# Kernel optimization log

Measured on AMD Instinct MI355X. Metric: run time of the kernel, lower is better.

Reference implementation:

```python
import jax, jax.numpy as jnp
import numpy as np

B, N, D, E = 64, 512, 256, 128   # batch, n_nodes, node_model_dim, edge_model_dim
N_ITERS = 20                      # max_iter_sinkhorn with fixed_n_iters=True


def setup_inputs() -> dict:
    key = jax.random.key(0)
    ks = jax.random.split(key, 9)
    return {
        "node_embeddings_inputs": jax.random.normal(ks[0], (B, N, D), jnp.float32),
        "node_masks_inputs": jax.random.randint(ks[1], (B, N), 0, 2).astype(bool),
        "node_embeddings_outputs": jax.random.normal(ks[2], (B, N, D), jnp.float32),
        # learned parameters
        "node_padding_features": jax.random.normal(ks[3], (1, 1, D), jnp.float32),
        "positional_encoding_outputs": jax.random.normal(ks[4], (1, N, D), jnp.float32),
        # stand-in for the (externally defined) EvoformerSetMatching pair stack:
        # a bilinear pair-affinity head, followed by the module's own linear_aff
        "W_a": jax.random.normal(ks[5], (D, E), jnp.float32) / np.sqrt(D),
        "W_b": jax.random.normal(ks[6], (D, E), jnp.float32) / np.sqrt(D),
        "w_aff": jax.random.normal(ks[7], (E,), jnp.float32) / np.sqrt(E),  # linear_aff weight
        "b_aff": jnp.zeros((), jnp.float32),                                # linear_aff bias
    }


def _sinkhorn(K, n_iters):
    # Fixed-iteration Sinkhorn projection toward a doubly-stochastic matrix:
    # alternately normalize columns (dim=2 sums) and rows (dim=1 sums).
    def step(P, _):
        P = P / jnp.sum(P, axis=2, keepdims=True)  # row-normalize over inputs axis
        P = P / jnp.sum(P, axis=1, keepdims=True)  # col-normalize over outputs axis
        return P, None
    P, _ = jax.lax.scan(step, K, None, length=n_iters)
    return P


def reference(node_embeddings_inputs, node_masks_inputs, node_embeddings_outputs,
              node_padding_features, positional_encoding_outputs,
              W_a, W_b, w_aff, b_aff):
    # replace padded input nodes with the learned padding feature
    mask = node_masks_inputs[..., None]                              # [B, N, 1]
    x_in = jnp.where(mask, node_padding_features, node_embeddings_inputs)
    # add positional encoding to output nodes (add_positionnal_outputs=True)
    x_out = node_embeddings_outputs + positional_encoding_outputs

    # pairwise affinity: aff[b, i(out), j(in)]  (linear_aff fused into the contraction
    # so the [B,N,N,E] pair tensor is never materialized)
    a = (x_out @ W_a) * w_aff                                        # [B, N, E]
    b = x_in @ W_b                                                   # [B, N, E]
    aff = jnp.einsum('bie,bje->bij', a, b) + b_aff                   # [B, N, N]

    # approximate doubly-stochastic init: average of the two marginal softmaxes
    K = 0.5 * jax.nn.softmax(aff, axis=1) + 0.5 * jax.nn.softmax(aff, axis=2)
    return _sinkhorn(K, N_ITERS)
```

## Files before the change

kernel.cpp:

```cpp
#include <hip/hip_runtime.h>
#include <cstddef>

static constexpr int CB = 64;
static constexpr int CN = 512;
static constexpr int CD = 256;
static constexpr int CE = 128;
static constexpr int CIT = 20;

typedef _Float16 half_t;
typedef __attribute__((ext_vector_type(8))) _Float16 v8h;
typedef __attribute__((ext_vector_type(4))) _Float16 v4h;
typedef __attribute__((ext_vector_type(4))) float v4f;

__global__ __launch_bounds__(512) void k0_init(
    const void* __restrict__ mask, int* __restrict__ flag,
    const float* __restrict__ W_a, const float* __restrict__ W_b,
    const float* __restrict__ w_aff,
    half_t* __restrict__ WaF, half_t* __restrict__ WbF,
    float4* __restrict__ clearp, int nclear4) {
  const int tid = threadIdx.x;
  const int blk = blockIdx.x;
  if (blk == 1) return;
  if (blk >= 18) {
    const int idx = (blk - 18) * 512 + tid;
    if (idx < nclear4)
      clearp[idx] = make_float4(-1.0f, -1.0f, -1.0f, -1.0f);
    return;
  }
  if (blk >= 2) {
    const bool is_a = (blk < 10);
    const float* W = is_a ? W_a : W_b;
    half_t* WF = is_a ? WaF : WbF;
    const int e = (blk - (is_a ? 2 : 10)) * 512 + tid;
    const int fB = e >> 6, lane = e & 63;
    const int nn = fB >> 3, kf = fB & 7;
    const int col = nn * 16 + (lane & 15);
    const int q = lane >> 4;
    const float scale = is_a ? w_aff[col] : 1.0f;
    v8h hv;
#pragma unroll
    for (int j = 0; j < 8; ++j) {
      const int k = kf * 32 + q * 8 + j;
      hv[j] = (half_t)(W[(size_t)k * CE + col] * scale);
    }
    *(v8h*)&WF[(size_t)e * 8] = hv;
    return;
  }
  __shared__ int cnt[5];
  if (tid < 5) cnt[tid] = 0;
  __syncthreads();
  const unsigned char* p = (const unsigned char*)mask;
  int l0 = 0, l1 = 0, l2 = 0, l3 = 0, l4 = 0;
  const int base = tid * 64;
  for (int k = 0; k < 64; ++k) {
    const int off = base + k;
    if (p[off]) {
      const int m4 = off & 3;
      if (m4 == 1) l1++;
      else if (m4 == 2) l2++;
      else if (m4 == 3) l3++;
      else if ((off & 7) == 4) l4++;
      else l0++;
    }
  }
  if (l0) atomicAdd(&cnt[0], 1);
  if (l1) atomicAdd(&cnt[1], 1);
  if (l2) atomicAdd(&cnt[2], 1);
  if (l3) atomicAdd(&cnt[3], 1);
  if (l4) atomicAdd(&cnt[4], 1);
  __syncthreads();
  if (tid == 0) {
    int f;
    if (cnt[1]) f = 1;
    else if (cnt[2] || cnt[3]) f = 2;
    else if (cnt[4]) f = 0;
    else if (cnt[0]) f = 3;
    else f = 1;
    *flag = f;
  }
}

__global__ __launch_bounds__(256) void prep_both(
    const float* __restrict__ out_emb, const float* __restrict__ pos,
    const float* __restrict__ in_emb, const float* __restrict__ pad,
    const void* __restrict__ maskp, const int* __restrict__ flagp,
    const half_t* __restrict__ WaF, const half_t* __restrict__ WbF,
    half_t* __restrict__ A_h, half_t* __restrict__ Bm_h) {
  __shared__ half_t Xs[64][264];
  const int tid = threadIdx.x;
  const int wv = tid >> 6, ln = tid & 63;
  const bool isA = blockIdx.x < 512;
  const int row0 = (isA ? blockIdx.x : blockIdx.x - 512) * 64;
  const float* X = isA ? out_emb : in_emb;
  const float* extra = isA ? pos : pad;
  const half_t* Wfrag = isA ? WaF : WbF;
  half_t* out = isA ? A_h : Bm_h;
  const int flag = isA ? 0 : *flagp;

#pragma unroll 4
  for (int it = 0; it < 16; ++it) {
    const int r = it * 4 + wv;
    const int row = row0 + r;
    const int c = ln * 4;
    float4 x4;
    if (isA) {
      x4 = *(const float4*)&X[(size_t)row * CD + c];
      const int i = row & (CN - 1);
      const float4 p4 = *(const float4*)&extra[(size_t)i * CD + c];
      x4.x += p4.x; x4.y += p4.y; x4.z += p4.z; x4.w += p4.w;
    } else {
      bool m;
      if (flag == 1)      m = ((const unsigned char*)maskp)[row] != 0;
      else if (flag == 2) m = ((const float*)maskp)[row] != 0.0f;
      else if (flag == 3) m = ((const long long*)maskp)[row] != 0;
      else                m = ((const int*)maskp)[row] != 0;
      if (m) x4 = *(const float4*)&extra[c];
      else   x4 = *(const float4*)&X[(size_t)row * CD + c];
    }
    v4h hv;
    hv[0] = (half_t)x4.x; hv[1] = (half_t)x4.y;
    hv[2] = (half_t)x4.z; hv[3] = (half_t)x4.w;
    *(v4h*)&Xs[r][c] = hv;
  }
  __syncthreads();

  const int q = ln >> 4, l = ln & 15;
  v8h af[8];
#pragma unroll
  for (int kf = 0; kf < 8; ++kf)
    af[kf] = *(v8h*)&Xs[wv * 16 + l][kf * 32 + q * 8];
  v4f acc[8] = {};
#pragma unroll
  for (int nn = 0; nn < 8; ++nn) {
    v8h bf[8];
#pragma unroll
    for (int kf = 0; kf < 8; ++kf)
      bf[kf] = *(const v8h*)&Wfrag[(size_t)((nn * 8 + kf) * 64 + ln) * 8];
#pragma unroll
    for (int kf = 0; kf < 8; ++kf)
      acc[nn] = __builtin_amdgcn_mfma_f32_16x16x32_f16(af[kf], bf[kf], acc[nn], 0, 0, 0);
  }
#pragma unroll
  for (int nn = 0; nn < 8; ++nn)
#pragma unroll
    for (int g = 0; g < 4; ++g) {
      const int row = row0 + wv * 16 + q * 4 + g;
      out[(size_t)row * CE + nn * 16 + l] = (half_t)acc[nn][g];
    }
}

__global__ __launch_bounds__(512, 2) void fused_reg(
    const half_t* __restrict__ A_h, const half_t* __restrict__ B_h,
    const float* __restrict__ baff, float* __restrict__ P,
    float* __restrict__ partInit, float* __restrict__ partIter) {
  __shared__ float comb2[8][512][2];
  __shared__ float2 w12[512];
  __shared__ float csinv_l[512];
  __shared__ float rinv_l[128];

  const int tid = threadIdx.x;
  const int wv = tid >> 6, ln = tid & 63;
  const int q = ln >> 4, l = ln & 15;
  const int b = blockIdx.x & 63;
  const int slab = blockIdx.x >> 6;
  const int i0 = slab * 128;
  const float bbs = *baff - 2.7725887f;

  int rs3[3];
  {
    int k = 0;
#pragma unroll
    for (int sl = 0; sl < 4; ++sl)
      if (sl != slab) rs3[k++] = sl;
  }

  v8h af[4];
  {
    const half_t* Arow = &A_h[((size_t)b * CN + i0 + wv * 16 + l) * CE];
#pragma unroll
    for (int ki = 0; ki < 4; ++ki)
      af[ki] = *(const v8h*)&Arow[ki * 32 + q * 8];
  }
  float ef[32][4];
  float d[4] = {0.0f, 0.0f, 0.0f, 0.0f};
  const half_t* Bbase = &B_h[(size_t)b * CN * CE];
#pragma unroll
  for (int ct = 0; ct < 32; ++ct) {
    v8h bf[4];
    const half_t* Brow = &Bbase[(size_t)(ct * 16 + l) * CE];
#pragma unroll
    for (int ki = 0; ki < 4; ++ki)
      bf[ki] = *(const v8h*)&Brow[ki * 32 + q * 8];
    v4f acc = {};
#pragma unroll
    for (int ki = 0; ki < 4; ++ki)
      acc = __builtin_amdgcn_mfma_f32_16x16x32_f16(af[ki], bf[ki], acc, 0, 0, 0);
    float colsum = 0.0f;
#pragma unroll
    for (int g = 0; g < 4; ++g) {
      const float e = __expf(acc[g] + bbs);
      ef[ct][g] = e;
      d[g] += e;
      colsum += e;
    }
    colsum += __shfl_xor(colsum, 16);
    colsum += __shfl_xor(colsum, 32);
    if (ln < 16) comb2[wv][ct * 16 + ln][0] = colsum;
  }
#pragma unroll
  for (int g = 0; g < 4; ++g) {
#pragma unroll
    for (int m = 1; m < 16; m <<= 1) d[g] += __shfl_xor(d[g], m);
  }
  if (l == 0) {
#pragma unroll
    for (int g = 0; g < 4; ++g) rinv_l[wv * 16 + q * 4 + g] = 1.0f / d[g];
  }
  __syncthreads();

  {
    float S = 0.0f;
#pragma unroll
    for (int w = 0; w < 8; ++w) S += comb2[w][tid][0];
    float T = S;
    __hip_atomic_store(&partInit[(((size_t)b * 4 + slab) * 512) + tid], S,
                       __ATOMIC_RELAXED, __HIP_MEMORY_SCOPE_AGENT);
    float v0, v1, v2;
    float* pb = &partInit[(size_t)b * 4 * 512];
    while (true) {
      v0 = __hip_atomic_load(&pb[rs3[0] * 512 + tid], __ATOMIC_RELAXED, __HIP_MEMORY_SCOPE_AGENT);
      v1 = __hip_atomic_load(&pb[rs3[1] * 512 + tid], __ATOMIC_RELAXED, __HIP_MEMORY_SCOPE_AGENT);
      v2 = __hip_atomic_load(&pb[rs3[2] * 512 + tid], __ATOMIC_RELAXED, __HIP_MEMORY_SCOPE_AGENT);
      if (v0 > 0.0f && v1 > 0.0f && v2 > 0.0f) break;
      __builtin_amdgcn_s_sleep(1);
    }
    T += v0 + v1 + v2;
    const float ci = 1.0f / T;
    csinv_l[tid] = ci;
    w12[tid] = make_float2(0.5f * ci, 1.0f);
  }
  float rv[4];
#pragma unroll
  for (int g = 0; g < 4; ++g) rv[g] = rinv_l[wv * 16 + q * 4 + g];

  float u_[4], uri[4];
  for (int t = 0; t < CIT; ++t) {
    __syncthreads();
    float p1[4] = {0, 0, 0, 0}, p2[4] = {0, 0, 0, 0};
#pragma unroll
    for (int ct = 0; ct < 32; ++ct) {
      const float2 w = w12[ct * 16 + l];
#pragma unroll
      for (int g = 0; g < 4; ++g) {
        const float e = ef[ct][g];
        p1[g] = fmaf(e, w.x, p1[g]);
        p2[g] = fmaf(e, w.y, p2[g]);
      }
    }
#pragma unroll
    for (int g = 0; g < 4; ++g) {
#pragma unroll
      for (int m = 1; m < 16; m <<= 1) {
        p1[g] += __shfl_xor(p1[g], m);
        p2[g] += __shfl_xor(p2[g], m);
      }
      u_[g] = 1.0f / (p1[g] + 0.5f * rv[g] * p2[g]);
      uri[g] = u_[g] * rv[g];
    }
#pragma unroll
    for (int ct = 0; ct < 32; ++ct) {
      float s1 = 0.0f, s2 = 0.0f;
#pragma unroll
      for (int g = 0; g < 4; ++g) {
        const float e = ef[ct][g];
        s1 = fmaf(e, u_[g], s1);
        s2 = fmaf(e, uri[g], s2);
      }
      s1 += __shfl_xor(s1, 16);
      s2 += __shfl_xor(s2, 16);
      const float sel = (ln >= 32) ? s1 : s2;
      const float recv = __shfl_xor(sel, 32);
      const float z = ((ln < 32) ? s1 : s2) + recv;
      if ((ln & 16) == 0) comb2[wv][ct * 16 + (ln & 15)][ln >> 5] = z;
    }
    __syncthreads();
    float S1 = 0.0f, S2 = 0.0f;
#pragma unroll
    for (int w = 0; w < 8; ++w) {
      const float2 c2 = *(const float2*)&comb2[w][tid][0];
      S1 += c2.x;
      S2 += c2.y;
    }
    const float ci = csinv_l[tid];
    const float Q = 0.5f * fmaf(ci, S1, S2);
    float* pr = &partIter[(((size_t)t * 64 + b) * 4) * 512];
    __hip_atomic_store(&pr[slab * 512 + tid], Q,
                       __ATOMIC_RELAXED, __HIP_MEMORY_SCOPE_AGENT);
    float v0, v1, v2;
    while (true) {
      v0 = __hip_atomic_load(&pr[rs3[0] * 512 + tid], __ATOMIC_RELAXED, __HIP_MEMORY_SCOPE_AGENT);
      v1 = __hip_atomic_load(&pr[rs3[1] * 512 + tid], __ATOMIC_RELAXED, __HIP_MEMORY_SCOPE_AGENT);
      v2 = __hip_atomic_load(&pr[rs3[2] * 512 + tid], __ATOMIC_RELAXED, __HIP_MEMORY_SCOPE_AGENT);
      if (v0 > 0.0f && v1 > 0.0f && v2 > 0.0f) break;
      __builtin_amdgcn_s_sleep(1);
    }
    const float vv = 1.0f / (Q + v0 + v1 + v2);
    w12[tid] = make_float2(0.5f * vv * ci, vv);
  }

  __syncthreads();
  float* Pb = &P[((size_t)b * CN + i0 + wv * 16 + q * 4) * CN];
#pragma unroll
  for (int ct = 0; ct < 32; ++ct) {
    const float2 w = w12[ct * 16 + l];
    const float c1 = w.x;
    const float c2 = 0.5f * w.y;
#pragma unroll
    for (int g = 0; g < 4; ++g) {
      const float e = ef[ct][g];
      Pb[(size_t)g * CN + ct * 16 + l] = e * fmaf(u_[g], c1, uri[g] * c2);
    }
  }
}

extern "C" void kernel_launch(void* const* d_in, const int* in_sizes, int n_in,
                              void* d_out, int out_size, void* d_ws, size_t ws_size,
                              hipStream_t stream) {
  const float* in_emb  = (const float*)d_in[0];
  const void*  mask    = d_in[1];
  const float* out_emb = (const float*)d_in[2];
  const float* pad     = (const float*)d_in[3];
  const float* pos     = (const float*)d_in[4];
  const float* W_a     = (const float*)d_in[5];
  const float* W_b     = (const float*)d_in[6];
  const float* w_aff   = (const float*)d_in[7];
  const float* b_aff   = (const float*)d_in[8];
  float* P = (float*)d_out;

  char* ws = (char*)d_ws;
  const size_t MB = 1024 * 1024;
  half_t* A_h  = (half_t*)ws;
  half_t* Bm_h = (half_t*)(ws + 8 * MB);
  int*    flag = (int*)(ws + 16 * MB);
  half_t* WaF  = (half_t*)(ws + 16 * MB + 16384);
  half_t* WbF  = (half_t*)(ws + 16 * MB + 16384 + 65536);
  float* partInit = (float*)(ws + 16 * MB + 256 * 1024);
  float* partIter = (float*)(ws + 16 * MB + 768 * 1024);

  const int nclear4 = (512 * 1024 + 10 * 1024 * 1024) / 16;
  const int nclrblk = (nclear4 + 511) / 512;

  k0_init<<<dim3(18 + nclrblk), dim3(512), 0, stream>>>(
      mask, flag, W_a, W_b, w_aff, WaF, WbF, (float4*)partInit, nclear4);
  prep_both<<<dim3(1024), dim3(256), 0, stream>>>(
      out_emb, pos, in_emb, pad, mask, flag, WaF, WbF, A_h, Bm_h);
  fused_reg<<<dim3(256), dim3(512), 0, stream>>>(
      A_h, Bm_h, b_aff, P, partInit, partIter);
}
```

Measured before the change: 309.6 us.

## Store exp tile in fp16 and do Sinkhorn reductions with MFMA

Keeps the exponentiated affinity tile in registers as fp16, plus a transposed copy computed with a second MFMA. Row and column sums in the init and in each Sinkhorn iteration become matrix-vector MFMAs against fp16 scaling vectors, replacing scalar FMA loops and cross-lane shuffle reductions. This cuts VALU and shuffle work per iteration, and fp16 storage halves the register footprint for the tile. In exchange it doubles the init MFMAs, wastes most MFMA output lanes because the operand is effectively a vector, and rounds the tile and scaling factors to fp16, which can hurt accuracy.

```diff
diff --git a/kernel.cpp b/kernel.cpp
--- a/kernel.cpp
+++ b/kernel.cpp
@@ -156,7 +156,8 @@
   __shared__ float comb2[8][512][2];
   __shared__ float2 w12[512];
   __shared__ float csinv_l[512];
-  __shared__ float rinv_l[128];
+  __shared__ half_t w1h[512];
+  __shared__ half_t w2h[512];
 
   const int tid = threadIdx.x;
   const int wv = tid >> 6, ln = tid & 63;
@@ -181,8 +182,8 @@
     for (int ki = 0; ki < 4; ++ki)
       af[ki] = *(const v8h*)&Arow[ki * 32 + q * 8];
   }
-  float ef[32][4];
-  float d[4] = {0.0f, 0.0f, 0.0f, 0.0f};
+  v4h eh[32];
+  v4h ehT[32];
   const half_t* Bbase = &B_h[(size_t)b * CN * CE];
 #pragma unroll
   for (int ct = 0; ct < 32; ++ct) {
@@ -191,31 +192,33 @@
 #pragma unroll
     for (int ki = 0; ki < 4; ++ki)
       bf[ki] = *(const v8h*)&Brow[ki * 32 + q * 8];
-    v4f acc = {};
-#pragma unroll
-    for (int ki = 0; ki < 4; ++ki)
-      acc = __builtin_amdgcn_mfma_f32_16x16x32_f16(af[ki], bf[ki], acc, 0, 0, 0);
-    float colsum = 0.0f;
+    v4f acc = {}, accT = {};
+#pragma unroll
+    for (int ki = 0; ki < 4; ++ki) {
+      acc  = __builtin_amdgcn_mfma_f32_16x16x32_f16(af[ki], bf[ki], acc,  0, 0, 0);
+      accT = __builtin_amdgcn_mfma_f32_16x16x32_f16(bf[ki], af[ki], accT, 0, 0, 0);
+    }
 #pragma unroll
     for (int g = 0; g < 4; ++g) {
-      const float e = __expf(acc[g] + bbs);
-      ef[ct][g] = e;
-      d[g] += e;
-      colsum += e;
-    }
-    colsum += __shfl_xor(colsum, 16);
-    colsum += __shfl_xor(colsum, 32);
-    if (ln < 16) comb2[wv][ct * 16 + ln][0] = colsum;
-  }
-#pragma unroll
-  for (int g = 0; g < 4; ++g) {
-#pragma unroll
-    for (int m = 1; m < 16; m <<= 1) d[g] += __shfl_xor(d[g], m);
-  }
-  if (l == 0) {
-#pragma unroll
-    for (int g = 0; g < 4; ++g) rinv_l[wv * 16 + q * 4 + g] = 1.0f / d[g];
-  }
+      eh[ct][g]  = (half_t)__expf(acc[g]  + bbs);
+      ehT[ct][g] = (half_t)__expf(accT[g] + bbs);
+    }
+  }
+
+  v4h ones;
+  ones[0] = (half_t)1.0f; ones[1] = (half_t)1.0f;
+  ones[2] = (half_t)1.0f; ones[3] = (half_t)1.0f;
+  v4f rowacc = {};
+#pragma unroll
+  for (int ct = 0; ct < 32; ++ct) {
+    const v4f c0 = __builtin_amdgcn_mfma_f32_16x16x16f16(ones, eh[ct], (v4f){}, 0, 0, 0);
+    if (ln < 16) comb2[wv][ct * 16 + ln][0] = c0[0];
+    rowacc = __builtin_amdgcn_mfma_f32_16x16x16f16(ones, ehT[ct], rowacc, 0, 0, 0);
+  }
+  float rv[4];
+#pragma unroll
+  for (int g = 0; g < 4; ++g)
+    rv[g] = 1.0f / __shfl(rowacc[0], q * 4 + g);
   __syncthreads();
 
   {
@@ -238,50 +241,36 @@
     const float ci = 1.0f / T;
     csinv_l[tid] = ci;
     w12[tid] = make_float2(0.5f * ci, 1.0f);
-  }
-  float rv[4];
-#pragma unroll
-  for (int g = 0; g < 4; ++g) rv[g] = rinv_l[wv * 16 + q * 4 + g];
+    w1h[tid] = (half_t)(0.5f * ci);
+    w2h[tid] = (half_t)1.0f;
+  }
 
   float u_[4], uri[4];
   for (int t = 0; t < CIT; ++t) {
     __syncthreads();
-    float p1[4] = {0, 0, 0, 0}, p2[4] = {0, 0, 0, 0};
+    v4f P1 = {}, P2 = {};
 #pragma unroll
     for (int ct = 0; ct < 32; ++ct) {
-      const float2 w = w12[ct * 16 + l];
-#pragma unroll
-      for (int g = 0; g < 4; ++g) {
-        const float e = ef[ct][g];
-        p1[g] = fmaf(e, w.x, p1[g]);
-        p2[g] = fmaf(e, w.y, p2[g]);
-      }
-    }
+      const v4h w1f = *(const v4h*)&w1h[ct * 16 + q * 4];
+      const v4h w2f = *(const v4h*)&w2h[ct * 16 + q * 4];
+      P1 = __builtin_amdgcn_mfma_f32_16x16x16f16(w1f, ehT[ct], P1, 0, 0, 0);
+      P2 = __builtin_amdgcn_mfma_f32_16x16x16f16(w2f, ehT[ct], P2, 0, 0, 0);
+    }
+    v4h u_h, uri_h;
 #pragma unroll
     for (int g = 0; g < 4; ++g) {
-#pragma unroll
-      for (int m = 1; m < 16; m <<= 1) {
-        p1[g] += __shfl_xor(p1[g], m);
-        p2[g] += __shfl_xor(p2[g], m);
-      }
-      u_[g] = 1.0f / (p1[g] + 0.5f * rv[g] * p2[g]);
+      const float p1 = __shfl(P1[0], q * 4 + g);
+      const float p2 = __shfl(P2[0], q * 4 + g);
+      u_[g] = 1.0f / (p1 + 0.5f * rv[g] * p2);
       uri[g] = u_[g] * rv[g];
+      u_h[g] = (half_t)u_[g];
+      uri_h[g] = (half_t)uri[g];
     }
 #pragma unroll
     for (int ct = 0; ct < 32; ++ct) {
-      float s1 = 0.0f, s2 = 0.0f;
-#pragma unroll
-      for (int g = 0; g < 4; ++g) {
-        const float e = ef[ct][g];
-        s1 = fmaf(e, u_[g], s1);
-        s2 = fmaf(e, uri[g], s2);
-      }
-      s1 += __shfl_xor(s1, 16);
-      s2 += __shfl_xor(s2, 16);
-      const float sel = (ln >= 32) ? s1 : s2;
-      const float recv = __shfl_xor(sel, 32);
-      const float z = ((ln < 32) ? s1 : s2) + recv;
-      if ((ln & 16) == 0) comb2[wv][ct * 16 + (ln & 15)][ln >> 5] = z;
+      const v4f sA = __builtin_amdgcn_mfma_f32_16x16x16f16(u_h,   eh[ct], (v4f){}, 0, 0, 0);
+      const v4f sB = __builtin_amdgcn_mfma_f32_16x16x16f16(uri_h, eh[ct], (v4f){}, 0, 0, 0);
+      if (ln < 32) comb2[wv][ct * 16 + (ln & 15)][ln >> 4] = (ln < 16) ? sA[0] : sB[0];
     }
     __syncthreads();
     float S1 = 0.0f, S2 = 0.0f;
@@ -306,6 +295,8 @@
     }
     const float vv = 1.0f / (Q + v0 + v1 + v2);
     w12[tid] = make_float2(0.5f * vv * ci, vv);
+    w1h[tid] = (half_t)(0.5f * vv * ci);
+    w2h[tid] = (half_t)vv;
   }
 
   __syncthreads();
@@ -317,7 +308,7 @@
     const float c2 = 0.5f * w.y;
 #pragma unroll
     for (int g = 0; g < 4; ++g) {
-      const float e = ef[ct][g];
+      const float e = (float)eh[ct][g];
       Pb[(size_t)g * CN + ct * 16 + l] = e * fmaf(u_[g], c1, uri[g] * c2);
     }
   }
```

After: 305.2 us. No clear change (-1.4%).
